# Kernel tuning notes

Hardware: AMD Instinct MI355X
Metric: run time of the kernel (lower is better)

Reference implementation:

```python
import jax, jax.numpy as jnp
import numpy as np

DIM = 768
NUM_HEADS = 12
N_TOKENS = 4096


def setup_inputs() -> dict:
    key = jax.random.key(0)
    k_x, k_qkv, k_proj, k_pb = jax.random.split(key, 4)
    x = jax.random.normal(k_x, (N_TOKENS, DIM), dtype=jnp.float32)
    # nn.Linear(dim, dim*3, bias=False): weight shape (3*dim, dim)
    w_qkv = jax.random.normal(k_qkv, (3 * DIM, DIM), dtype=jnp.float32) * (DIM ** -0.5)
    # nn.Linear(dim, dim): weight (dim, dim), bias (dim,)
    w_proj = jax.random.normal(k_proj, (DIM, DIM), dtype=jnp.float32) * (DIM ** -0.5)
    b_proj = jax.random.normal(k_pb, (DIM,), dtype=jnp.float32) * 0.01
    return {"x": x, "w_qkv": w_qkv, "w_proj": w_proj, "b_proj": b_proj}


def reference(x, w_qkv, w_proj, b_proj):
    N, C = x.shape
    H = NUM_HEADS
    hd = C // H
    scale = hd ** -0.5
    qkv = (x @ w_qkv.T).reshape(N, 3, H, hd)  # (N, 3, H, hd)
    q = qkv[:, 0]  # (N, H, hd)
    k = qkv[:, 1]
    v = qkv[:, 2]
    # full NxN score matrix per head, as in the original (non-flash) code
    attn = jnp.einsum("nhd,mhd->hnm", q, k) * scale  # (H, N, N)
    attn = jax.nn.softmax(attn, axis=-1)
    out = jnp.einsum("hnm,mhd->nhd", attn, v).reshape(N, C)  # (N, C)
    return out @ w_proj.T + b_proj
```

## Files before the change

kernel.cpp:

```cpp
#include <hip/hip_runtime.h>
#include <hip/hip_bf16.h>

typedef __bf16 bf16_t;
typedef __attribute__((ext_vector_type(8))) __bf16 bf16x8;
typedef __attribute__((ext_vector_type(4))) __bf16 bf16x4;
typedef __attribute__((ext_vector_type(4))) short s16x4;
typedef __attribute__((ext_vector_type(4))) float f32x4;

#define NTOK 4096
#define DIM  768
#define NH   12
#define HD   64
#define NSPLIT 2
#define KHALF (NTOK / NSPLIT)
#define XSZ  (NTOK * DIM)
#define WQSZ (3 * DIM * DIM)
#define WPSZ (DIM * DIM)
#define SCALE_L2E 0.18033688011112042f
#define SOFTMAX_C 12.0f
#define KSTR 72
#define VSTR 74

__device__ __forceinline__ bf16x8 load8(const bf16_t* p) {
    return *reinterpret_cast<const bf16x8*>(p);
}
__device__ __forceinline__ void store8(bf16_t* p, bf16x8 v) {
    *reinterpret_cast<bf16x8*>(p) = v;
}
__device__ __forceinline__ void gl2lds16(const bf16_t* g, bf16_t* l) {
    __builtin_amdgcn_global_load_lds(
        (const __attribute__((address_space(1))) void*)g,
        (__attribute__((address_space(3))) void*)l, 16, 0, 0);
}

__global__ __launch_bounds__(256) void cvt_kernel(
    const float* __restrict__ x, const float* __restrict__ wq,
    const float* __restrict__ wp,
    bf16_t* __restrict__ xb, bf16_t* __restrict__ wqb, bf16_t* __restrict__ wpb)
{
    size_t i = ((size_t)blockIdx.x * 256 + threadIdx.x) * 4;
    const float* src; bf16_t* dst; size_t off;
    if (i < XSZ)             { src = x;  dst = xb;  off = i; }
    else if (i < XSZ + WQSZ) { src = wq; dst = wqb; off = i - XSZ; }
    else                     { src = wp; dst = wpb; off = i - XSZ - WQSZ; }
    float4 v = *reinterpret_cast<const float4*>(src + off);
    bf16x4 o = { (bf16_t)v.x, (bf16_t)v.y, (bf16_t)v.z, (bf16_t)v.w };
    *reinterpret_cast<bf16x4*>(dst + off) = o;
}

__global__ __launch_bounds__(256) void qkv_gemm_kernel(
    const bf16_t* __restrict__ X, const bf16_t* __restrict__ W,
    bf16_t* __restrict__ Qo, bf16_t* __restrict__ Ko, bf16_t* __restrict__ Vt)
{
    __shared__ __align__(16) bf16_t As[128 * 32];
    __shared__ __align__(16) bf16_t Bs[128 * 32];
    const int tid  = threadIdx.x;
    const int wave = tid >> 6, lane = tid & 63;
    const int lr = lane & 15, lq = lane >> 4;
    const int M0 = blockIdx.x * 128;
    const int N0 = blockIdx.y * 128;
    const int wm = (wave >> 1) * 64, wn = (wave & 1) * 64;

    const int g_row = wave * 32 + (lane >> 2);
    const int g_col = (lane & 3) * 8;

    f32x4 acc[4][4] = {};

    for (int k0 = 0; k0 < DIM; k0 += 32) {
        #pragma unroll
        for (int c = 0; c < 2; ++c) {
            gl2lds16(&X[(size_t)(M0 + g_row + c * 16) * DIM + k0 + g_col],
                     &As[(wave * 32 + c * 16) * 32]);
            gl2lds16(&W[(size_t)(N0 + g_row + c * 16) * DIM + k0 + g_col],
                     &Bs[(wave * 32 + c * 16) * 32]);
        }
        __syncthreads();
        bf16x8 af[4], bfr[4];
        #pragma unroll
        for (int i = 0; i < 4; ++i) af[i]  = load8(&As[(wm + i * 16 + lr) * 32 + lq * 8]);
        #pragma unroll
        for (int i = 0; i < 4; ++i) bfr[i] = load8(&Bs[(wn + i * 16 + lr) * 32 + lq * 8]);
        #pragma unroll
        for (int r = 0; r < 4; ++r)
            #pragma unroll
            for (int c = 0; c < 4; ++c)
                acc[r][c] = __builtin_amdgcn_mfma_f32_16x16x32_bf16(af[r], bfr[c], acc[r][c], 0, 0, 0);
        __syncthreads();
    }

    const int t = N0 / DIM;
    if (t == 2) {
        #pragma unroll
        for (int r = 0; r < 4; ++r)
            #pragma unroll
            for (int c = 0; c < 4; ++c) {
                int m0 = M0 + wm + r * 16 + lq * 4;
                int rem = N0 + wn + c * 16 + lr - 2 * DIM;
                int hh = rem >> 6, d = rem & 63;
                bf16x4 v = { (bf16_t)acc[r][c][0], (bf16_t)acc[r][c][1],
                             (bf16_t)acc[r][c][2], (bf16_t)acc[r][c][3] };
                *reinterpret_cast<bf16x4*>(&Vt[((size_t)hh * HD + d) * NTOK + m0]) = v;
            }
    } else {
        #pragma unroll
        for (int r = 0; r < 4; ++r)
            #pragma unroll
            for (int c = 0; c < 4; ++c)
                #pragma unroll
                for (int reg = 0; reg < 4; ++reg) {
                    int m = M0 + wm + r * 16 + lq * 4 + reg;
                    int rem = N0 + wn + c * 16 + lr - t * DIM;
                    int hh = rem >> 6, d = rem & 63;
                    float v = acc[r][c][reg];
                    if (t == 0) Qo[(hh * NTOK + m) * HD + d] = (bf16_t)(v * SCALE_L2E);
                    else        Ko[(hh * NTOK + m) * HD + d] = (bf16_t)v;
                }
    }
}

__global__ __launch_bounds__(256) void flash_attn_kernel(
    const bf16_t* __restrict__ Qb, const bf16_t* __restrict__ Kb,
    const bf16_t* __restrict__ Vtb, float* __restrict__ Opart,
    float* __restrict__ Lpart)
{
    __shared__ __align__(16) bf16_t Ks[2][64 * KSTR];
    __shared__ __align__(16) bf16_t Vs[2][64 * VSTR];
    const int tid  = threadIdx.x;
    const int wave = tid >> 6, lane = tid & 63;
    const int lr = lane & 15, lq = lane >> 4;
    const int h  = blockIdx.y;
    const int q0 = blockIdx.x * 128;
    const int sp = blockIdx.z;
    const int kt0 = sp * KHALF;
    const int NIT = KHALF / 64;

    const bf16_t* qrowA = &Qb[((size_t)h * NTOK + q0 + wave * 32 + lr) * HD];
    const bf16_t* qrowB = qrowA + 16 * HD;
    bf16x8 qa0 = load8(&qrowA[lq * 8]);
    bf16x8 qa1 = load8(&qrowA[32 + lq * 8]);
    bf16x8 qb0 = load8(&qrowB[lq * 8]);
    bf16x8 qb1 = load8(&qrowB[32 + lq * 8]);

    float la = 0.f, lb = 0.f;
    f32x4 oA[4] = {}, oB[4] = {};

    const int srA = tid >> 3;
    const int scA = (tid & 7) * 8;
    const bf16_t* kbase = &Kb[(size_t)h * NTOK * HD];
    const bf16_t* vbase = &Vtb[(size_t)h * HD * NTOK];

    bf16x8 pk0 = load8(&kbase[(size_t)(kt0 + srA) * HD + scA]);
    bf16x8 pk1 = load8(&kbase[(size_t)(kt0 + srA + 32) * HD + scA]);
    bf16x8 pv0 = load8(&vbase[(size_t)srA * NTOK + kt0 + scA]);
    bf16x8 pv1 = load8(&vbase[(size_t)(srA + 32) * NTOK + kt0 + scA]);

    for (int it = 0; it < NIT; ++it) {
        const int kt  = kt0 + it * 64;
        const int buf = it & 1;
        store8(&Ks[buf][srA * KSTR + scA],        pk0);
        store8(&Ks[buf][(srA + 32) * KSTR + scA], pk1);
        store8(&Vs[buf][srA * VSTR + scA],        pv0);
        store8(&Vs[buf][(srA + 32) * VSTR + scA], pv1);
        __syncthreads();

        if (it + 1 < NIT) {
            const int kn = kt + 64;
            pk0 = load8(&kbase[(size_t)(kn + srA) * HD + scA]);
            pk1 = load8(&kbase[(size_t)(kn + srA + 32) * HD + scA]);
            pv0 = load8(&vbase[(size_t)srA * NTOK + kn + scA]);
            pv1 = load8(&vbase[(size_t)(srA + 32) * NTOK + kn + scA]);
        }

        f32x4 sa[4], sb[4];
        #pragma unroll
        for (int g = 0; g < 4; ++g) {
            bf16x8 k0 = load8(&Ks[buf][(g * 16 + lr) * KSTR + lq * 8]);
            bf16x8 k1 = load8(&Ks[buf][(g * 16 + lr) * KSTR + 32 + lq * 8]);
            f32x4 za = {}, zb = {};
            za = __builtin_amdgcn_mfma_f32_16x16x32_bf16(k0, qa0, za, 0, 0, 0);
            za = __builtin_amdgcn_mfma_f32_16x16x32_bf16(k1, qa1, za, 0, 0, 0);
            zb = __builtin_amdgcn_mfma_f32_16x16x32_bf16(k0, qb0, zb, 0, 0, 0);
            zb = __builtin_amdgcn_mfma_f32_16x16x32_bf16(k1, qb1, zb, 0, 0, 0);
            sa[g] = za; sb[g] = zb;
        }

        #pragma unroll
        for (int g = 0; g < 4; ++g)
            #pragma unroll
            for (int r = 0; r < 4; ++r) {
                sa[g][r] = __builtin_amdgcn_exp2f(sa[g][r] - SOFTMAX_C);
                la += sa[g][r];
                sb[g][r] = __builtin_amdgcn_exp2f(sb[g][r] - SOFTMAX_C);
                lb += sb[g][r];
            }

        #pragma unroll
        for (int g = 0; g < 4; ++g) {
            bf16x4 pa = { (bf16_t)sa[g][0], (bf16_t)sa[g][1],
                          (bf16_t)sa[g][2], (bf16_t)sa[g][3] };
            bf16x4 pb = { (bf16_t)sb[g][0], (bf16_t)sb[g][1],
                          (bf16_t)sb[g][2], (bf16_t)sb[g][3] };
            s16x4 psa = __builtin_bit_cast(s16x4, pa);
            s16x4 psb = __builtin_bit_cast(s16x4, pb);
            #pragma unroll
            for (int dt = 0; dt < 4; ++dt) {
                s16x4 va = *reinterpret_cast<const s16x4*>(
                    &Vs[buf][(dt * 16 + lr) * VSTR + g * 16 + lq * 4]);
                oA[dt] = __builtin_amdgcn_mfma_f32_16x16x16bf16_1k(va, psa, oA[dt], 0, 0, 0);
                oB[dt] = __builtin_amdgcn_mfma_f32_16x16x16bf16_1k(va, psb, oB[dt], 0, 0, 0);
            }
        }
    }

    la += __shfl_xor(la, 16); la += __shfl_xor(la, 32);
    lb += __shfl_xor(lb, 16); lb += __shfl_xor(lb, 32);
    const int ma = q0 + wave * 32 + lr;
    const int mb = ma + 16;
    if (lq == 0) {
        Lpart[((size_t)sp * NH + h) * NTOK + ma] = la;
        Lpart[((size_t)sp * NH + h) * NTOK + mb] = lb;
    }
    float* oa = &Opart[((size_t)sp * NTOK + ma) * DIM + h * HD];
    float* ob = &Opart[((size_t)sp * NTOK + mb) * DIM + h * HD];
    #pragma unroll
    for (int dt = 0; dt < 4; ++dt) {
        *reinterpret_cast<f32x4*>(&oa[dt * 16 + lq * 4]) = oA[dt];
        *reinterpret_cast<f32x4*>(&ob[dt * 16 + lq * 4]) = oB[dt];
    }
}

__global__ __launch_bounds__(256) void proj_gemm_kernel(
    const float* __restrict__ Opart, const float* __restrict__ Lpart,
    const bf16_t* __restrict__ W, const float* __restrict__ bias,
    float* __restrict__ out)
{
    __shared__ __align__(16) bf16_t As[64 * 40];
    __shared__ __align__(16) bf16_t Bs[64 * 40];
    const int tid  = threadIdx.x;
    const int wave = tid >> 6, lane = tid & 63;
    const int lr = lane & 15, lq = lane >> 4;
    const int M0 = blockIdx.x * 64;
    const int N0 = blockIdx.y * 64;
    const int srow = tid >> 2, scol = (tid & 3) * 8;
    const int wr = (wave >> 1) * 32, wc = (wave & 1) * 32;
    const int am = M0 + srow;

    f32x4 acc[2][2] = {};

    for (int k0 = 0; k0 < DIM; k0 += 32) {
        const int col = k0 + scol;
        const int hh = col >> 6;
        float l = Lpart[(size_t)hh * NTOK + am]
                + Lpart[(size_t)(NH + hh) * NTOK + am];
        float rv = 1.f / l;
        const float* p0 = &Opart[(size_t)am * DIM + col];
        const float* p1 = &Opart[(size_t)(NTOK + am) * DIM + col];
        f32x4 x0 = *reinterpret_cast<const f32x4*>(p0);
        f32x4 x1 = *reinterpret_cast<const f32x4*>(p0 + 4);
        f32x4 y0 = *reinterpret_cast<const f32x4*>(p1);
        f32x4 y1 = *reinterpret_cast<const f32x4*>(p1 + 4);
        bf16x8 a;
        #pragma unroll
        for (int j = 0; j < 4; ++j) {
            a[j]     = (bf16_t)((x0[j] + y0[j]) * rv);
            a[j + 4] = (bf16_t)((x1[j] + y1[j]) * rv);
        }
        store8(&As[srow * 40 + scol], a);
        store8(&Bs[srow * 40 + scol], load8(&W[(size_t)(N0 + srow) * DIM + col]));
        __syncthreads();
        bf16x8 a0 = load8(&As[(wr + lr) * 40 + lq * 8]);
        bf16x8 a1 = load8(&As[(wr + 16 + lr) * 40 + lq * 8]);
        bf16x8 b0 = load8(&Bs[(wc + lr) * 40 + lq * 8]);
        bf16x8 b1 = load8(&Bs[(wc + 16 + lr) * 40 + lq * 8]);
        acc[0][0] = __builtin_amdgcn_mfma_f32_16x16x32_bf16(a0, b0, acc[0][0], 0, 0, 0);
        acc[0][1] = __builtin_amdgcn_mfma_f32_16x16x32_bf16(a0, b1, acc[0][1], 0, 0, 0);
        acc[1][0] = __builtin_amdgcn_mfma_f32_16x16x32_bf16(a1, b0, acc[1][0], 0, 0, 0);
        acc[1][1] = __builtin_amdgcn_mfma_f32_16x16x32_bf16(a1, b1, acc[1][1], 0, 0, 0);
        __syncthreads();
    }

    #pragma unroll
    for (int r = 0; r < 2; ++r)
        #pragma unroll
        for (int c = 0; c < 2; ++c)
            #pragma unroll
            for (int reg = 0; reg < 4; ++reg) {
                int m = M0 + wr + r * 16 + lq * 4 + reg;
                int n = N0 + wc + c * 16 + lr;
                out[(size_t)m * DIM + n] = acc[r][c][reg] + bias[n];
            }
}

extern "C" void kernel_launch(void* const* d_in, const int* in_sizes, int n_in,
                              void* d_out, int out_size, void* d_ws, size_t ws_size,
                              hipStream_t stream)
{
    const float* x      = (const float*)d_in[0];
    const float* w_qkv  = (const float*)d_in[1];
    const float* w_proj = (const float*)d_in[2];
    const float* b_proj = (const float*)d_in[3];
    float* out = (float*)d_out;

    char* ws = (char*)d_ws;
    const size_t sz = (size_t)NH * NTOK * HD * sizeof(bf16_t);
    bf16_t* Q     = (bf16_t*)(ws);
    bf16_t* K     = (bf16_t*)(ws + sz);
    bf16_t* Vt    = (bf16_t*)(ws + 2 * sz);
    bf16_t* xb    = (bf16_t*)(ws + 3 * sz);
    bf16_t* wqb   = (bf16_t*)(ws + 3 * sz + (size_t)XSZ * 2);
    bf16_t* wpb   = (bf16_t*)(ws + 3 * sz + (size_t)(XSZ + WQSZ) * 2);
    char*   ws2   = ws + 3 * sz + (size_t)(XSZ + WQSZ + WPSZ) * 2;
    float*  Opart = (float*)ws2;
    float*  Lpart = (float*)(ws2 + (size_t)NSPLIT * NTOK * DIM * 4);

    cvt_kernel<<<dim3((XSZ + WQSZ + WPSZ) / 1024), 256, 0, stream>>>(
        x, w_qkv, w_proj, xb, wqb, wpb);
    qkv_gemm_kernel<<<dim3(NTOK / 128, (3 * DIM) / 128), 256, 0, stream>>>(
        xb, wqb, Q, K, Vt);
    flash_attn_kernel<<<dim3(NTOK / 128, NH, NSPLIT), 256, 0, stream>>>(
        Q, K, Vt, Opart, Lpart);
    proj_gemm_kernel<<<dim3(NTOK / 64, DIM / 64), 256, 0, stream>>>(
        Opart, Lpart, wpb, b_proj, out);
}
```

Before: 211.5 us.

## Swizzle attention LDS tiles, fold softmax offset into MFMA init, split combine kernel

```diff
diff --git a/kernel.cpp b/kernel.cpp
--- a/kernel.cpp
+++ b/kernel.cpp
@@ -18,8 +18,6 @@
 #define WPSZ (DIM * DIM)
 #define SCALE_L2E 0.18033688011112042f
 #define SOFTMAX_C 12.0f
-#define KSTR 72
-#define VSTR 74
 
 __device__ __forceinline__ bf16x8 load8(const bf16_t* p) {
     return *reinterpret_cast<const bf16x8*>(p);
@@ -118,13 +116,13 @@
     }
 }
 
-__global__ __launch_bounds__(256) void flash_attn_kernel(
+__global__ __launch_bounds__(256, 5) void flash_attn_kernel(
     const bf16_t* __restrict__ Qb, const bf16_t* __restrict__ Kb,
     const bf16_t* __restrict__ Vtb, float* __restrict__ Opart,
     float* __restrict__ Lpart)
 {
-    __shared__ __align__(16) bf16_t Ks[2][64 * KSTR];
-    __shared__ __align__(16) bf16_t Vs[2][64 * VSTR];
+    __shared__ __align__(16) bf16_t Ks[2][64 * 64];
+    __shared__ __align__(16) bf16_t Vs[2][64 * 64];
     const int tid  = threadIdx.x;
     const int wave = tid >> 6, lane = tid & 63;
     const int lr = lane & 15, lq = lane >> 4;
@@ -134,6 +132,14 @@
     const int kt0 = sp * KHALF;
     const int NIT = KHALF / 64;
 
+    const int sw_st = ((tid & 7) ^ ((tid >> 3) & 7)) * 8;
+    const int kc0   = (lq ^ (lr & 7)) * 8;
+    const int kc1   = ((4 + lq) ^ (lr & 7)) * 8;
+    int vc[4];
+    #pragma unroll
+    for (int g = 0; g < 4; ++g)
+        vc[g] = ((2 * g + (lq >> 1)) ^ (lr & 7)) * 8 + (lq & 1) * 4;
+
     const bf16_t* qrowA = &Qb[((size_t)h * NTOK + q0 + wave * 32 + lr) * HD];
     const bf16_t* qrowB = qrowA + 16 * HD;
     bf16x8 qa0 = load8(&qrowA[lq * 8]);
@@ -143,6 +149,7 @@
 
     float la = 0.f, lb = 0.f;
     f32x4 oA[4] = {}, oB[4] = {};
+    const f32x4 mc = { -SOFTMAX_C, -SOFTMAX_C, -SOFTMAX_C, -SOFTMAX_C };
 
     const int srA = tid >> 3;
     const int scA = (tid & 7) * 8;
@@ -157,10 +164,10 @@
     for (int it = 0; it < NIT; ++it) {
         const int kt  = kt0 + it * 64;
         const int buf = it & 1;
-        store8(&Ks[buf][srA * KSTR + scA],        pk0);
-        store8(&Ks[buf][(srA + 32) * KSTR + scA], pk1);
-        store8(&Vs[buf][srA * VSTR + scA],        pv0);
-        store8(&Vs[buf][(srA + 32) * VSTR + scA], pv1);
+        store8(&Ks[buf][srA * 64 + sw_st],        pk0);
+        store8(&Ks[buf][(srA + 32) * 64 + sw_st], pk1);
+        store8(&Vs[buf][srA * 64 + sw_st],        pv0);
+        store8(&Vs[buf][(srA + 32) * 64 + sw_st], pv1);
         __syncthreads();
 
         if (it + 1 < NIT) {
@@ -172,28 +179,31 @@
         }
 
         f32x4 sa[4], sb[4];
+        __builtin_amdgcn_s_setprio(1);
         #pragma unroll
         for (int g = 0; g < 4; ++g) {
-            bf16x8 k0 = load8(&Ks[buf][(g * 16 + lr) * KSTR + lq * 8]);
-            bf16x8 k1 = load8(&Ks[buf][(g * 16 + lr) * KSTR + 32 + lq * 8]);
-            f32x4 za = {}, zb = {};
+            bf16x8 k0 = load8(&Ks[buf][(g * 16 + lr) * 64 + kc0]);
+            bf16x8 k1 = load8(&Ks[buf][(g * 16 + lr) * 64 + kc1]);
+            f32x4 za = mc, zb = mc;
             za = __builtin_amdgcn_mfma_f32_16x16x32_bf16(k0, qa0, za, 0, 0, 0);
             za = __builtin_amdgcn_mfma_f32_16x16x32_bf16(k1, qa1, za, 0, 0, 0);
             zb = __builtin_amdgcn_mfma_f32_16x16x32_bf16(k0, qb0, zb, 0, 0, 0);
             zb = __builtin_amdgcn_mfma_f32_16x16x32_bf16(k1, qb1, zb, 0, 0, 0);
             sa[g] = za; sb[g] = zb;
         }
+        __builtin_amdgcn_s_setprio(0);
 
         #pragma unroll
         for (int g = 0; g < 4; ++g)
             #pragma unroll
             for (int r = 0; r < 4; ++r) {
-                sa[g][r] = __builtin_amdgcn_exp2f(sa[g][r] - SOFTMAX_C);
+                sa[g][r] = __builtin_amdgcn_exp2f(sa[g][r]);
                 la += sa[g][r];
-                sb[g][r] = __builtin_amdgcn_exp2f(sb[g][r] - SOFTMAX_C);
+                sb[g][r] = __builtin_amdgcn_exp2f(sb[g][r]);
                 lb += sb[g][r];
             }
 
+        __builtin_amdgcn_s_setprio(1);
         #pragma unroll
         for (int g = 0; g < 4; ++g) {
             bf16x4 pa = { (bf16_t)sa[g][0], (bf16_t)sa[g][1],
@@ -205,11 +215,12 @@
             #pragma unroll
             for (int dt = 0; dt < 4; ++dt) {
                 s16x4 va = *reinterpret_cast<const s16x4*>(
-                    &Vs[buf][(dt * 16 + lr) * VSTR + g * 16 + lq * 4]);
+                    &Vs[buf][(dt * 16 + lr) * 64 + vc[g]]);
                 oA[dt] = __builtin_amdgcn_mfma_f32_16x16x16bf16_1k(va, psa, oA[dt], 0, 0, 0);
                 oB[dt] = __builtin_amdgcn_mfma_f32_16x16x16bf16_1k(va, psb, oB[dt], 0, 0, 0);
             }
         }
+        __builtin_amdgcn_s_setprio(0);
     }
 
     la += __shfl_xor(la, 16); la += __shfl_xor(la, 32);
@@ -229,49 +240,56 @@
     }
 }
 
+__global__ __launch_bounds__(256) void combine_kernel(
+    const float* __restrict__ Opart, const float* __restrict__ Lpart,
+    bf16_t* __restrict__ Ab)
+{
+    int idx = blockIdx.x * 256 + threadIdx.x;
+    int m = idx / (DIM / 4);
+    int c = (idx - m * (DIM / 4)) * 4;
+    int hh = c >> 6;
+    float l = 0.f;
+    #pragma unroll
+    for (int s = 0; s < NSPLIT; ++s)
+        l += Lpart[((size_t)s * NH + hh) * NTOK + m];
+    float rv = 1.f / l;
+    float a0 = 0.f, a1 = 0.f, a2 = 0.f, a3 = 0.f;
+    #pragma unroll
+    for (int s = 0; s < NSPLIT; ++s) {
+        f32x4 v = *reinterpret_cast<const f32x4*>(
+            &Opart[((size_t)s * NTOK + m) * DIM + c]);
+        a0 += v[0]; a1 += v[1]; a2 += v[2]; a3 += v[3];
+    }
+    bf16x4 o = { (bf16_t)(a0 * rv), (bf16_t)(a1 * rv),
+                 (bf16_t)(a2 * rv), (bf16_t)(a3 * rv) };
+    *reinterpret_cast<bf16x4*>(&Ab[(size_t)m * DIM + c]) = o;
+}
+
 __global__ __launch_bounds__(256) void proj_gemm_kernel(
-    const float* __restrict__ Opart, const float* __restrict__ Lpart,
-    const bf16_t* __restrict__ W, const float* __restrict__ bias,
-    float* __restrict__ out)
-{
-    __shared__ __align__(16) bf16_t As[64 * 40];
-    __shared__ __align__(16) bf16_t Bs[64 * 40];
+    const bf16_t* __restrict__ A, const bf16_t* __restrict__ W,
+    const float* __restrict__ bias, float* __restrict__ out)
+{
+    __shared__ __align__(16) bf16_t As[64 * 32];
+    __shared__ __align__(16) bf16_t Bs[64 * 32];
     const int tid  = threadIdx.x;
     const int wave = tid >> 6, lane = tid & 63;
     const int lr = lane & 15, lq = lane >> 4;
     const int M0 = blockIdx.x * 64;
     const int N0 = blockIdx.y * 64;
-    const int srow = tid >> 2, scol = (tid & 3) * 8;
     const int wr = (wave >> 1) * 32, wc = (wave & 1) * 32;
-    const int am = M0 + srow;
+    const int g_row = tid >> 2;
+    const int g_col = (tid & 3) * 8;
 
     f32x4 acc[2][2] = {};
 
     for (int k0 = 0; k0 < DIM; k0 += 32) {
-        const int col = k0 + scol;
-        const int hh = col >> 6;
-        float l = Lpart[(size_t)hh * NTOK + am]
-                + Lpart[(size_t)(NH + hh) * NTOK + am];
-        float rv = 1.f / l;
-        const float* p0 = &Opart[(size_t)am * DIM + col];
-        const float* p1 = &Opart[(size_t)(NTOK + am) * DIM + col];
-        f32x4 x0 = *reinterpret_cast<const f32x4*>(p0);
-        f32x4 x1 = *reinterpret_cast<const f32x4*>(p0 + 4);
-        f32x4 y0 = *reinterpret_cast<const f32x4*>(p1);
-        f32x4 y1 = *reinterpret_cast<const f32x4*>(p1 + 4);
-        bf16x8 a;
-        #pragma unroll
-        for (int j = 0; j < 4; ++j) {
-            a[j]     = (bf16_t)((x0[j] + y0[j]) * rv);
-            a[j + 4] = (bf16_t)((x1[j] + y1[j]) * rv);
-        }
-        store8(&As[srow * 40 + scol], a);
-        store8(&Bs[srow * 40 + scol], load8(&W[(size_t)(N0 + srow) * DIM + col]));
-        __syncthreads();
-        bf16x8 a0 = load8(&As[(wr + lr) * 40 + lq * 8]);
-        bf16x8 a1 = load8(&As[(wr + 16 + lr) * 40 + lq * 8]);
-        bf16x8 b0 = load8(&Bs[(wc + lr) * 40 + lq * 8]);
-        bf16x8 b1 = load8(&Bs[(wc + 16 + lr) * 40 + lq * 8]);
+        gl2lds16(&A[(size_t)(M0 + g_row) * DIM + k0 + g_col], &As[wave * 512]);
+        gl2lds16(&W[(size_t)(N0 + g_row) * DIM + k0 + g_col], &Bs[wave * 512]);
+        __syncthreads();
+        bf16x8 a0 = load8(&As[(wr + lr) * 32 + lq * 8]);
+        bf16x8 a1 = load8(&As[(wr + 16 + lr) * 32 + lq * 8]);
+        bf16x8 b0 = load8(&Bs[(wc + lr) * 32 + lq * 8]);
+        bf16x8 b1 = load8(&Bs[(wc + 16 + lr) * 32 + lq * 8]);
         acc[0][0] = __builtin_amdgcn_mfma_f32_16x16x32_bf16(a0, b0, acc[0][0], 0, 0, 0);
         acc[0][1] = __builtin_amdgcn_mfma_f32_16x16x32_bf16(a0, b1, acc[0][1], 0, 0, 0);
         acc[1][0] = __builtin_amdgcn_mfma_f32_16x16x32_bf16(a1, b0, acc[1][0], 0, 0, 0);
@@ -312,6 +330,7 @@
     char*   ws2   = ws + 3 * sz + (size_t)(XSZ + WQSZ + WPSZ) * 2;
     float*  Opart = (float*)ws2;
     float*  Lpart = (float*)(ws2 + (size_t)NSPLIT * NTOK * DIM * 4);
+    bf16_t* Ab    = xb;
 
     cvt_kernel<<<dim3((XSZ + WQSZ + WPSZ) / 1024), 256, 0, stream>>>(
         x, w_qkv, w_proj, xb, wqb, wpb);
@@ -319,6 +338,8 @@
         xb, wqb, Q, K, Vt);
     flash_attn_kernel<<<dim3(NTOK / 128, NH, NSPLIT), 256, 0, stream>>>(
         Q, K, Vt, Opart, Lpart);
+    combine_kernel<<<dim3((NTOK * DIM / 4) / 256), 256, 0, stream>>>(
+        Opart, Lpart, Ab);
     proj_gemm_kernel<<<dim3(NTOK / 64, DIM / 64), 256, 0, stream>>>(
-        Opart, Lpart, wpb, b_proj, out);
-}
+        Ab, wpb, b_proj, out);
+}
```

Measured after the change: 340.9 us. 1.61x slower.
